# Kernel tuning notes

Measured on AMD Instinct MI355X. Metric: run time of the kernel, lower is better.

Reference implementation:

```python
import jax, jax.numpy as jnp
import numpy as np

NUM_Q_HEADS = 64
NUM_KV_HEADS = 8
HEAD_DIM = 64
HIDDEN = 2880
SLIDING_WINDOW = 128
ROPE_WAVELENGTH = 10000.0
NEG_INF = jnp.float32(-1e9)


def _rope(x, start_index=0):
    # x: (b, s, n, h). yarn with scaling_factor=1.0 == standard RoPE (split-half rotate).
    s, h = x.shape[1], x.shape[-1]
    inv_freq = 1.0 / (ROPE_WAVELENGTH ** (jnp.arange(0, h, 2, dtype=jnp.float32) / h))
    pos = jnp.arange(s, dtype=jnp.float32) + start_index
    freqs = pos[:, None] * inv_freq[None, :]  # (s, h/2)
    cos = jnp.concatenate([jnp.cos(freqs), jnp.cos(freqs)], axis=-1)[None, :, None, :]
    sin = jnp.concatenate([jnp.sin(freqs), jnp.sin(freqs)], axis=-1)[None, :, None, :]
    x1, x2 = jnp.split(x, 2, axis=-1)
    rot = jnp.concatenate([-x2, x1], axis=-1)
    return x * cos + rot * sin


def setup_inputs() -> dict:
    key = jax.random.key(0)
    ks = jax.random.split(key, 9)
    b, s = 1, 2048
    scale = 0.02
    hidden_states = jax.random.normal(ks[0], (b, s, HIDDEN), jnp.float32)
    Wq = jax.random.normal(ks[1], (HIDDEN, NUM_Q_HEADS, HEAD_DIM), jnp.float32) * scale
    Wk = jax.random.normal(ks[2], (HIDDEN, NUM_KV_HEADS, HEAD_DIM), jnp.float32) * scale
    Wv = jax.random.normal(ks[3], (HIDDEN, NUM_KV_HEADS, HEAD_DIM), jnp.float32) * scale
    Wo = jax.random.normal(ks[4], (NUM_Q_HEADS, HEAD_DIM, HIDDEN), jnp.float32) * scale
    bq = jnp.zeros((NUM_Q_HEADS, HEAD_DIM), jnp.float32)
    bk = jnp.zeros((NUM_KV_HEADS, HEAD_DIM), jnp.float32)
    bv = jnp.zeros((NUM_KV_HEADS, HEAD_DIM), jnp.float32)
    bo = jnp.zeros((HIDDEN,), jnp.float32)
    sinks = jax.random.normal(ks[5], (NUM_Q_HEADS,), jnp.float32) * 0.05
    attention_mask = jnp.tril(jnp.ones((s, s), bool))[None]  # causal, (b, q, k)
    return dict(hidden_states=hidden_states, Wq=Wq, bq=bq, Wk=Wk, bk=bk, Wv=Wv,
                bv=bv, Wo=Wo, bo=bo, sinks=sinks, attention_mask=attention_mask)


def reference(hidden_states, Wq, bq, Wk, bk, Wv, bv, Wo, bo, sinks, attention_mask):
    b, s, _ = hidden_states.shape
    inv_norm = 1.0 / np.sqrt(HEAD_DIM).astype(np.float32)
    # QKV projections (EinsumDense with bias)
    q = jnp.einsum('bqm,muh->bquh', hidden_states, Wq) + bq
    k = jnp.einsum('bkm,mvh->bkvh', hidden_states, Wk) + bk
    v = jnp.einsum('bkm,mvh->bkvh', hidden_states, Wv) + bv
    # rotary_dim == head_dim (even), so RoPE applies to the full head dim
    q = _rope(q)
    k = _rope(k)
    # GQA: repeat kv heads
    groups = NUM_Q_HEADS // NUM_KV_HEADS
    k = jnp.repeat(k, groups, axis=2)
    v = jnp.repeat(v, groups, axis=2)
    scores = jnp.einsum('bquh,bkuh->buqk', q, k) * inv_norm
    # sliding-window mask: keep kv_pos >= q_pos - window
    qpos = jnp.arange(s)
    swin = qpos[None, :] >= qpos[:, None] - SLIDING_WINDOW  # (q, k)
    scores = jnp.where(swin[None, None], scores, NEG_INF)
    scores = jnp.where(attention_mask[:, None], scores, NEG_INF)
    # sink-token logit per head appended as extra kv column
    sink = jnp.broadcast_to(sinks.reshape(1, NUM_Q_HEADS, 1, 1), (b, NUM_Q_HEADS, s, 1))
    logits = jnp.concatenate([scores, sink], axis=-1)
    m = jax.lax.stop_gradient(jnp.max(logits, axis=-1, keepdims=True))
    probs = jax.nn.softmax(logits - m, axis=-1)[..., :-1]  # drop sink column
    attn = jnp.einsum('buqk,bkuh->bquh', probs, v)
    return jnp.einsum('bquh,uhm->bqm', attn, Wo) + bo
```

## Files before the change

kernel.cpp:

```cpp
#include <hip/hip_runtime.h>
#include <cstdint>

typedef __attribute__((ext_vector_type(4))) float f32x4;
typedef __attribute__((ext_vector_type(8))) short bf16x8;

#define HIDDEN 2880
#define SEQ 2048
#define QKV_N 5120
#define WIN 128

__device__ __forceinline__ ushort f2bf(float f) {
  uint32_t u = __builtin_bit_cast(uint32_t, f);
  u += 0x7fff + ((u >> 16) & 1);
  return (ushort)(u >> 16);
}
__device__ __forceinline__ float bf2f(ushort h) {
  uint32_t u = ((uint32_t)h) << 16;
  return __builtin_bit_cast(float, u);
}

__global__ void conv_kernel(const float* __restrict__ in, ushort* __restrict__ out, int n) {
  int i = (blockIdx.x * blockDim.x + threadIdx.x) * 8;
  if (i >= n) return;
  float4 a = *(const float4*)(in + i);
  float4 b = *(const float4*)(in + i + 4);
  bf16x8 o;
  o[0] = (short)f2bf(a.x); o[1] = (short)f2bf(a.y); o[2] = (short)f2bf(a.z); o[3] = (short)f2bf(a.w);
  o[4] = (short)f2bf(b.x); o[5] = (short)f2bf(b.y); o[6] = (short)f2bf(b.z); o[7] = (short)f2bf(b.w);
  *(bf16x8*)(out + i) = o;
}

__global__ __launch_bounds__(256) void tconv2_kernel(const float* __restrict__ in, ushort* __restrict__ out,
                                                     int C, int out_ld, int out_row_off) {
  __shared__ ushort tile[64][68];
  int c0 = blockIdx.x * 64, r0 = blockIdx.y * 64;
  int t = threadIdx.x;
  int lr = t >> 4;
  int lc = (t & 15) * 4;
#pragma unroll
  for (int i = 0; i < 4; ++i) {
    float4 v = *(const float4*)&in[(size_t)(r0 + i * 16 + lr) * C + c0 + lc];
    ushort4 o;
    o.x = f2bf(v.x); o.y = f2bf(v.y); o.z = f2bf(v.z); o.w = f2bf(v.w);
    *(ushort4*)&tile[i * 16 + lr][lc] = o;
  }
  __syncthreads();
  int rr0 = (t & 7) * 8;
#pragma unroll
  for (int i2 = 0; i2 < 2; ++i2) {
    int cc = i2 * 32 + (t >> 3);
    bf16x8 o;
#pragma unroll
    for (int j = 0; j < 8; ++j) o[j] = (short)tile[rr0 + j][cc];
    *(bf16x8*)&out[(size_t)(out_row_off + c0 + cc) * out_ld + r0 + rr0] = o;
  }
}

__global__ void biascat_kernel(const float* __restrict__ bq, const float* __restrict__ bk,
                               const float* __restrict__ bv, float* __restrict__ out) {
  int i = blockIdx.x * blockDim.x + threadIdx.x;
  if (i >= QKV_N) return;
  float v = (i < 4096) ? bq[i] : (i < 4608) ? bk[i - 4096] : bv[i - 4608];
  out[i] = v;
}

__global__ void ropetab_kernel(float2* __restrict__ tab) {
  int i = blockIdx.x * blockDim.x + threadIdx.x;
  int s = i >> 5, d = i & 31;
  float inv = powf(10000.0f, -(float)d / 32.0f);
  float f = (float)s * inv;
  tab[i] = make_float2(cosf(f), sinf(f));
}

__global__ __launch_bounds__(256) void vt_kernel(const ushort* __restrict__ qkv, ushort* __restrict__ vt) {
  __shared__ ushort tile[64][80];
  int kv0 = blockIdx.x * 64, d0 = blockIdx.y * 64;
  int t = threadIdx.x;
#pragma unroll
  for (int p = 0; p < 2; ++p) {
    int lr = p * 32 + (t >> 3);
    *(bf16x8*)&tile[lr][(t & 7) * 8] =
        *(const bf16x8*)&qkv[(size_t)(kv0 + lr) * QKV_N + 4608 + d0 + (t & 7) * 8];
  }
  __syncthreads();
#pragma unroll
  for (int p = 0; p < 2; ++p) {
    int dl = p * 32 + (t >> 3);
    bf16x8 o;
#pragma unroll
    for (int jj = 0; jj < 8; ++jj) o[jj] = (short)tile[(t & 7) * 8 + jj][dl];
    *(bf16x8*)&vt[(size_t)(d0 + dl) * 2048 + kv0 + (t & 7) * 8] = o;
  }
}

template <int BN, bool OUT_BF16>
__global__ __launch_bounds__(256, 2) void gemm4w_kernel(
    const ushort* __restrict__ A, const ushort* __restrict__ Bt,
    const float* __restrict__ bias, void* __restrict__ Cv,
    int K, int lda, int ldb, int ldc) {
  constexpr int NFRAG = BN / 32;
  constexpr int BHALF = BN * 64;
  constexpr int BCHUNKS = BHALF / 1024;
  constexpr int BUFBYTES = 16384 + 2 * BHALF;
  __shared__ __align__(16) char ldsbuf[2 * BUFBYTES];

  const int cpx = gridDim.x >> 3;
  const int wg = ((int)blockIdx.x & 7) * cpx + ((int)blockIdx.x >> 3);
  const int mtile = wg & 15, ntile = wg >> 4;
  const int m0 = mtile * 128, n0 = ntile * BN;

  const int tid = threadIdx.x, wv = tid >> 6, l = tid & 63;
  const int wm = wv >> 1, wn = wv & 1;
  const int r = l & 15, g = l >> 4;

  const int c = l ^ ((l >> 3) & 3);
  const ushort* gA0 = A + (size_t)(m0 + (c >> 2)) * lda + (c & 3) * 8;
  const ushort* gB0 = Bt + (size_t)(n0 + (c >> 2)) * ldb + (c & 3) * 8;

  const int gsw = (g * 16) ^ (((r >> 1) & 3) << 4);
  const int aOff = (wm * 64 + r) * 64 + gsw;
  const int bOff = (wn * (NFRAG * 16) + r) * 64 + gsw;

  auto sA = [&](int nb, int kg, int kh) {
#pragma unroll
    for (int j = 0; j < 2; ++j) {
      int cid = j * 4 + wv;
      __builtin_amdgcn_global_load_lds(
          (const __attribute__((address_space(1))) void*)(const void*)(gA0 + (size_t)cid * 16 * lda + kg),
          (__attribute__((address_space(3))) void*)&ldsbuf[nb * BUFBYTES + kh * 8192 + cid * 1024], 16, 0, 0);
    }
  };
  auto sB = [&](int nb, int kg, int kh) {
#pragma unroll
    for (int j = 0; j < (BCHUNKS + 3) / 4; ++j) {
      int cid = j * 4 + wv;
      if (cid < BCHUNKS)
        __builtin_amdgcn_global_load_lds(
            (const __attribute__((address_space(1))) void*)(const void*)(gB0 + (size_t)cid * 16 * ldb + kg),
            (__attribute__((address_space(3))) void*)&ldsbuf[nb * BUFBYTES + 16384 + kh * BHALF + cid * 1024],
            16, 0, 0);
    }
  };

#define BAR() __builtin_amdgcn_s_barrier()
#define LGKMC(N)                                                       \
  do {                                                                 \
    asm volatile("s_waitcnt lgkmcnt(%0)" ::"n"(N) : "memory");         \
    __builtin_amdgcn_sched_barrier(0);                                 \
  } while (0)
#define WAITV0() asm volatile("s_waitcnt vmcnt(0)" ::: "memory")

  f32x4 acc[4][NFRAG] = {};
  const int nt = K >> 6;

  sA(0, 0, 0); sA(0, 32, 1); sB(0, 0, 0); sB(0, 32, 1);
  WAITV0();
  BAR();

  for (int t = 0; t < nt; ++t) {
    const int bufOff = (t & 1) * BUFBYTES;
    const int nb = (t & 1) ^ 1;
    bf16x8 aq0[4], bq0[NFRAG], aq1[4], bq1[NFRAG];
#pragma unroll
    for (int nf = 0; nf < NFRAG; ++nf)
      bq0[nf] = *(const bf16x8*)&ldsbuf[bufOff + 16384 + bOff + nf * 1024];
#pragma unroll
    for (int mi = 0; mi < 4; ++mi)
      aq0[mi] = *(const bf16x8*)&ldsbuf[bufOff + aOff + mi * 1024];
    __builtin_amdgcn_sched_barrier(0);
#pragma unroll
    for (int nf = 0; nf < NFRAG; ++nf)
      bq1[nf] = *(const bf16x8*)&ldsbuf[bufOff + 16384 + BHALF + bOff + nf * 1024];
#pragma unroll
    for (int mi = 0; mi < 4; ++mi)
      aq1[mi] = *(const bf16x8*)&ldsbuf[bufOff + 8192 + aOff + mi * 1024];
    if (t + 1 < nt) {
      const int kn = (t + 1) * 64;
      sA(nb, kn, 0); sA(nb, kn + 32, 1);
      sB(nb, kn, 0); sB(nb, kn + 32, 1);
    }
    LGKMC(4 + NFRAG);
    __builtin_amdgcn_s_setprio(1);
#pragma unroll
    for (int mi = 0; mi < 4; ++mi)
#pragma unroll
      for (int nf = 0; nf < NFRAG; ++nf)
        acc[mi][nf] = __builtin_amdgcn_mfma_f32_16x16x32_bf16(aq0[mi], bq0[nf], acc[mi][nf], 0, 0, 0);
    __builtin_amdgcn_s_setprio(0);
    LGKMC(0);
    __builtin_amdgcn_s_setprio(1);
#pragma unroll
    for (int mi = 0; mi < 4; ++mi)
#pragma unroll
      for (int nf = 0; nf < NFRAG; ++nf)
        acc[mi][nf] = __builtin_amdgcn_mfma_f32_16x16x32_bf16(aq1[mi], bq1[nf], acc[mi][nf], 0, 0, 0);
    __builtin_amdgcn_s_setprio(0);
    WAITV0();
    BAR();
  }

#pragma unroll
  for (int mf2 = 0; mf2 < 4; ++mf2) {
#pragma unroll
    for (int nf = 0; nf < NFRAG; ++nf) {
      int cc = n0 + wn * (NFRAG * 16) + nf * 16 + r;
      float b = bias[cc];
#pragma unroll
      for (int j = 0; j < 4; ++j) {
        int rrow = m0 + wm * 64 + mf2 * 16 + g * 4 + j;
        float v = acc[mf2][nf][j] + b;
        if (OUT_BF16) ((ushort*)Cv)[(size_t)rrow * ldc + cc] = f2bf(v);
        else ((float*)Cv)[(size_t)rrow * ldc + cc] = v;
      }
    }
  }
#undef BAR
#undef LGKMC
#undef WAITV0
}

__global__ __launch_bounds__(512, 4) void attn_kernel(
    const ushort* __restrict__ qkv, const ushort* __restrict__ vt,
    const float* __restrict__ sinks, const float2* __restrict__ tab,
    ushort* __restrict__ out) {
  __shared__ __align__(16) char lds[54272];
  const int kh = blockIdx.y;
  const int q0 = blockIdx.x * 32;
  const int kvw0 = q0 - 128;
  const int tid = threadIdx.x, w = tid >> 6, l = tid & 63;
  const int r = l & 15, g = l >> 4;
  const int h = kh * 8 + w;

  if (tid < 256) ((uint32_t*)(lds + 40960))[tid] = 0;

#pragma unroll
  for (int it = 0; it < 4; ++it) {
    int c = it * 512 + tid;
    if (c < 640) {
      int row = c >> 2, ch = c & 3;
      int kv = kvw0 + row;
      bf16x8 v1 = {}, v2 = {};
      if (kv >= 0) {
        const ushort* kb = &qkv[(size_t)kv * QKV_N + 4096 + kh * 64 + ch * 8];
        bf16x8 x1 = *(const bf16x8*)kb;
        bf16x8 x2 = *(const bf16x8*)(kb + 32);
#pragma unroll
        for (int i = 0; i < 8; ++i) {
          float2 cs = tab[(kv << 5) + ch * 8 + i];
          float a = bf2f((ushort)x1[i]), b = bf2f((ushort)x2[i]);
          v1[i] = (short)f2bf(a * cs.x - b * cs.y);
          v2[i] = (short)f2bf(b * cs.x + a * cs.y);
        }
      }
      int b1 = (row * 128 + ch * 16) ^ ((row & 7) << 4);
      int b2 = (row * 128 + (ch + 4) * 16) ^ ((row & 7) << 4);
      *(bf16x8*)(lds + b1) = v1;
      *(bf16x8*)(lds + b2) = v2;
    } else if (c < 1920) {
      int cv = c - 640;
      int row = cv / 20, ch = cv - (cv / 20) * 20;
      int kv = kvw0 + ch * 8;
      bf16x8 vv = {};
      if (kv >= 0) vv = *(const bf16x8*)&vt[(size_t)(kh * 64 + row) * 2048 + kv];
      int byte = (row * 320 + ch * 16) ^ ((row & 7) << 4);
      *(bf16x8*)(lds + 20480 + byte) = vv;
    }
  }
  __syncthreads();

  char* Pw = lds + 41984 + w * 1536;
  const float snk = sinks[h];

#pragma unroll
  for (int si = 0; si < 2; ++si) {
    const ushort* qb = &qkv[(size_t)(q0 + si * 16 + r) * QKV_N + h * 64 + g * 8];
    bf16x8 qf0 = *(const bf16x8*)qb;
    bf16x8 qf1 = *(const bf16x8*)(qb + 32);
    {
      int s = q0 + si * 16 + r;
      bf16x8 t0, t1;
#pragma unroll
      for (int i = 0; i < 8; ++i) {
        float2 cs = tab[(s << 5) + g * 8 + i];
        float a = bf2f((ushort)qf0[i]), b = bf2f((ushort)qf1[i]);
        t0[i] = (short)f2bf(a * cs.x - b * cs.y);
        t1[i] = (short)f2bf(b * cs.x + a * cs.y);
      }
      qf0 = t0; qf1 = t1;
    }

    f32x4 S[9];
    float mx[4] = {-3e30f, -3e30f, -3e30f, -3e30f};
#pragma unroll
    for (int tt = 0; tt < 9; ++tt) {
      int kvloc = (si + tt) * 16 + r;
      int b0 = (kvloc * 128 + g * 16) ^ ((kvloc & 7) << 4);
      int b1 = (kvloc * 128 + 64 + g * 16) ^ ((kvloc & 7) << 4);
      bf16x8 kf0 = *(const bf16x8*)(lds + b0);
      bf16x8 kf1 = *(const bf16x8*)(lds + b1);
      f32x4 s = {};
      s = __builtin_amdgcn_mfma_f32_16x16x32_bf16(qf0, kf0, s, 0, 0, 0);
      s = __builtin_amdgcn_mfma_f32_16x16x32_bf16(qf1, kf1, s, 0, 0, 0);
      int kvc = kvw0 + kvloc;
#pragma unroll
      for (int j = 0; j < 4; ++j) {
        int qr = q0 + si * 16 + g * 4 + j;
        bool valid = (kvc >= 0) && (kvc <= qr) && (kvc >= qr - WIN);
        float v = valid ? s[j] * 0.125f : -1e30f;
        s[j] = v;
        mx[j] = fmaxf(mx[j], v);
      }
      S[tt] = s;
    }
#pragma unroll
    for (int off = 1; off < 16; off <<= 1)
#pragma unroll
      for (int j = 0; j < 4; ++j) mx[j] = fmaxf(mx[j], __shfl_xor(mx[j], off, 64));
    float m[4], sum[4] = {0, 0, 0, 0};
#pragma unroll
    for (int j = 0; j < 4; ++j) m[j] = fmaxf(mx[j], snk);
#pragma unroll
    for (int tt = 0; tt < 9; ++tt)
#pragma unroll
      for (int j = 0; j < 4; ++j) {
        float p = (S[tt][j] > -1e29f) ? __expf(S[tt][j] - m[j]) : 0.0f;
        S[tt][j] = p;
        sum[j] += p;
      }
#pragma unroll
    for (int off = 1; off < 16; off <<= 1)
#pragma unroll
      for (int j = 0; j < 4; ++j) sum[j] += __shfl_xor(sum[j], off, 64);
    float rinv[4];
#pragma unroll
    for (int j = 0; j < 4; ++j) rinv[j] = 1.0f / (sum[j] + __expf(snk - m[j]));

    f32x4 acc[4] = {};
#pragma unroll
    for (int ks = 0; ks < 5; ++ks) {
#pragma unroll
      for (int c2 = 0; c2 < 2; ++c2) {
        int tt = 2 * ks + c2;
#pragma unroll
        for (int j = 0; j < 4; ++j) {
          float pv = (tt <= 8) ? S[tt][j] * rinv[j] : 0.0f;
          *(ushort*)(Pw + ((g * 4 + j) * 48 + c2 * 16 + r) * 2) = f2bf(pv);
        }
      }
      bf16x8 pa = *(const bf16x8*)(Pw + (r * 48 + g * 8) * 2);
#pragma unroll
      for (int ni = 0; ni < 4; ++ni) {
        int row = ni * 16 + r;
        int byte = (row * 320 + (si * 16 + ks * 32 + g * 8) * 2) ^ ((row & 7) << 4);
        bf16x8 vb = *(const bf16x8*)(lds + 20480 + byte);
        acc[ni] = __builtin_amdgcn_mfma_f32_16x16x32_bf16(pa, vb, acc[ni], 0, 0, 0);
      }
    }
#pragma unroll
    for (int ni = 0; ni < 4; ++ni)
#pragma unroll
      for (int j = 0; j < 4; ++j)
        out[(size_t)(q0 + si * 16 + g * 4 + j) * 4096 + h * 64 + ni * 16 + r] = f2bf(acc[ni][j]);
  }
}

extern "C" void kernel_launch(void* const* d_in, const int* in_sizes, int n_in,
                              void* d_out, int out_size, void* d_ws, size_t ws_size,
                              hipStream_t stream) {
  const float* hs = (const float*)d_in[0];
  const float* Wq = (const float*)d_in[1];
  const float* bq = (const float*)d_in[2];
  const float* Wk = (const float*)d_in[3];
  const float* bk = (const float*)d_in[4];
  const float* Wv = (const float*)d_in[5];
  const float* bv = (const float*)d_in[6];
  const float* Wo = (const float*)d_in[7];
  const float* bo = (const float*)d_in[8];
  const float* sinks = (const float*)d_in[9];
  float* out = (float*)d_out;

  char* ws = (char*)d_ws;
  ushort* hs_bf   = (ushort*)(ws + 0);
  ushort* vt_g    = (ushort*)(ws + 0);
  ushort* wqkv_t  = (ushort*)(ws + 11796480);
  ushort* attn    = (ushort*)(ws + 11796480);
  ushort* wo_t    = (ushort*)(ws + 41287680);
  ushort* qkv     = (ushort*)(ws + 66453504);
  float*  bias_all= (float*)(ws + 87425024);
  float2* tab     = (float2*)(ws + 87445504);

  conv_kernel<<<5898240 / 8 / 256, 256, 0, stream>>>(hs, hs_bf, 5898240);
  tconv2_kernel<<<dim3(64, 45), 256, 0, stream>>>(Wq, wqkv_t, 4096, 2880, 0);
  tconv2_kernel<<<dim3(8, 45), 256, 0, stream>>>(Wk, wqkv_t, 512, 2880, 4096);
  tconv2_kernel<<<dim3(8, 45), 256, 0, stream>>>(Wv, wqkv_t, 512, 2880, 4608);
  tconv2_kernel<<<dim3(45, 64), 256, 0, stream>>>(Wo, wo_t, 2880, 4096, 0);
  biascat_kernel<<<20, 256, 0, stream>>>(bq, bk, bv, bias_all);
  ropetab_kernel<<<2048 * 32 / 256, 256, 0, stream>>>(tab);

  gemm4w_kernel<160, true><<<512, 256, 0, stream>>>(hs_bf, wqkv_t, bias_all, qkv,
                                                    2880, 2880, 2880, 5120);
  vt_kernel<<<dim3(32, 8), 256, 0, stream>>>(qkv, vt_g);
  attn_kernel<<<dim3(64, 8), 512, 0, stream>>>(qkv, vt_g, sinks, tab, attn);
  gemm4w_kernel<192, false><<<240, 256, 0, stream>>>(attn, wo_t, bo, out,
                                                     4096, 4096, 4096, 2880);
}
```

Measured before the change: 202.7 us.

## Add intra-block split-K GEMM for QKV projection and retune output GEMM tiles

Adds a new 512-thread QKV projection GEMM with 128x320 tiles. Its 8 waves are split into two K-halves, and the two partial sums are reduced through LDS before the bias add and bf16 store, which halves the grid to 256 blocks of larger tiles. The output projection GEMM moves from BN=192 with 240 blocks to BN=160 with 288 blocks. The generic GEMM's inner loop is also restructured to load and compute each K-half in turn with a full LDS wait, replacing the previous partial-wait overlap. The aim is better data reuse and CU balance, at the cost of the LDS reduction step and possibly less overlap between LDS loads and MFMA.

Result: slower. 212.1 us (+4.6%).

```diff
diff --git a/kernel.cpp b/kernel.cpp
--- a/kernel.cpp
+++ b/kernel.cpp
@@ -90,6 +90,131 @@
 #pragma unroll
     for (int jj = 0; jj < 8; ++jj) o[jj] = (short)tile[(t & 7) * 8 + jj][dl];
     *(bf16x8*)&vt[(size_t)(d0 + dl) * 2048 + kv0 + (t & 7) * 8] = o;
+  }
+}
+
+#define LGKM0()                                              \
+  do {                                                       \
+    asm volatile("s_waitcnt lgkmcnt(0)" ::: "memory");       \
+    __builtin_amdgcn_sched_barrier(0);                       \
+  } while (0)
+#define WAITV0() asm volatile("s_waitcnt vmcnt(0)" ::: "memory")
+#define BAR() __builtin_amdgcn_s_barrier()
+
+__global__ __launch_bounds__(512, 2) void gemmks_kernel(
+    const ushort* __restrict__ A, const ushort* __restrict__ Bt,
+    const float* __restrict__ bias, ushort* __restrict__ Cv,
+    int K, int lda, int ldb, int ldc) {
+  constexpr int BUFBYTES = 57344;
+  __shared__ __align__(16) char ldsbuf[2 * BUFBYTES];
+
+  const int cpx = gridDim.x >> 3;
+  const int wg = ((int)blockIdx.x & 7) * cpx + ((int)blockIdx.x >> 3);
+  const int mtile = wg & 15, ntile = wg >> 4;
+  const int m0 = mtile * 128, n0 = ntile * 320;
+
+  const int tid = threadIdx.x, wv = tid >> 6, l = tid & 63;
+  const int wn = wv & 3, wk = wv >> 2;
+  const int r = l & 15, g = l >> 4;
+
+  const int c = l ^ ((l >> 3) & 3);
+  const ushort* gA0 = A + (size_t)(m0 + (c >> 2)) * lda + (c & 3) * 8;
+  const ushort* gB0 = Bt + (size_t)(n0 + (c >> 2)) * ldb + (c & 3) * 8;
+
+  const int gsw = (g * 16) ^ (((r >> 1) & 3) << 4);
+  const int aOff = r * 64 + gsw;
+  const int bOff = (wn * 80 + r) * 64 + gsw;
+
+  auto sA = [&](int nb, int kg) {
+#pragma unroll
+    for (int j = 0; j < 2; ++j) {
+      int cid = wv * 2 + j;
+      int kh = cid >> 3, rc = cid & 7;
+      __builtin_amdgcn_global_load_lds(
+          (const __attribute__((address_space(1))) void*)(const void*)(gA0 + (size_t)rc * 16 * lda + kg + kh * 32),
+          (__attribute__((address_space(3))) void*)&ldsbuf[nb * BUFBYTES + kh * 8192 + rc * 1024], 16, 0, 0);
+    }
+  };
+  auto sB = [&](int nb, int kg) {
+#pragma unroll
+    for (int j = 0; j < 5; ++j) {
+      int cid = wv * 5 + j;
+      int kh = cid / 20, cc = cid - (cid / 20) * 20;
+      __builtin_amdgcn_global_load_lds(
+          (const __attribute__((address_space(1))) void*)(const void*)(gB0 + (size_t)cc * 16 * ldb + kg + kh * 32),
+          (__attribute__((address_space(3))) void*)&ldsbuf[nb * BUFBYTES + 16384 + kh * 20480 + cc * 1024],
+          16, 0, 0);
+    }
+  };
+
+  f32x4 acc[8][5] = {};
+  const int nt = K >> 6;
+
+  sA(0, 0); sB(0, 0);
+  WAITV0();
+  BAR();
+
+  for (int t = 0; t < nt; ++t) {
+    const int bufOff = (t & 1) * BUFBYTES;
+    const int nb = (t & 1) ^ 1;
+    bf16x8 aq[8], bq[5];
+    const int khA = bufOff + wk * 8192;
+    const int khB = bufOff + 16384 + wk * 20480;
+#pragma unroll
+    for (int nf = 0; nf < 5; ++nf)
+      bq[nf] = *(const bf16x8*)&ldsbuf[khB + bOff + nf * 1024];
+#pragma unroll
+    for (int mi = 0; mi < 8; ++mi)
+      aq[mi] = *(const bf16x8*)&ldsbuf[khA + aOff + mi * 1024];
+    if (t + 1 < nt) { sA(nb, (t + 1) * 64); sB(nb, (t + 1) * 64); }
+    LGKM0();
+    __builtin_amdgcn_s_setprio(1);
+#pragma unroll
+    for (int mi = 0; mi < 8; ++mi)
+#pragma unroll
+      for (int nf = 0; nf < 5; ++nf)
+        acc[mi][nf] = __builtin_amdgcn_mfma_f32_16x16x32_bf16(aq[mi], bq[nf], acc[mi][nf], 0, 0, 0);
+    __builtin_amdgcn_s_setprio(0);
+    WAITV0();
+    BAR();
+  }
+
+#pragma unroll
+  for (int ch = 0; ch < 2; ++ch) {
+    if (wk == 1) {
+#pragma unroll
+      for (int mi = 0; mi < 4; ++mi)
+#pragma unroll
+        for (int nf = 0; nf < 5; ++nf)
+          *(f32x4*)&ldsbuf[wn * 20480 + (mi * 5 + nf) * 1024 + l * 16] = acc[ch * 4 + mi][nf];
+    }
+    __syncthreads();
+    if (wk == 0) {
+#pragma unroll
+      for (int mi = 0; mi < 4; ++mi)
+#pragma unroll
+        for (int nf = 0; nf < 5; ++nf) {
+          f32x4 o = *(const f32x4*)&ldsbuf[wn * 20480 + (mi * 5 + nf) * 1024 + l * 16];
+#pragma unroll
+          for (int j = 0; j < 4; ++j) acc[ch * 4 + mi][nf][j] += o[j];
+        }
+    }
+    __syncthreads();
+  }
+
+  if (wk == 0) {
+#pragma unroll
+    for (int mi = 0; mi < 8; ++mi)
+#pragma unroll
+      for (int nf = 0; nf < 5; ++nf) {
+        int cc = n0 + wn * 80 + nf * 16 + r;
+        float b = bias[cc];
+#pragma unroll
+        for (int j = 0; j < 4; ++j) {
+          int rrow = m0 + mi * 16 + g * 4 + j;
+          Cv[(size_t)rrow * ldc + cc] = f2bf(acc[mi][nf][j] + b);
+        }
+      }
   }
 }
 
@@ -142,14 +267,6 @@
     }
   };
 
-#define BAR() __builtin_amdgcn_s_barrier()
-#define LGKMC(N)                                                       \
-  do {                                                                 \
-    asm volatile("s_waitcnt lgkmcnt(%0)" ::"n"(N) : "memory");         \
-    __builtin_amdgcn_sched_barrier(0);                                 \
-  } while (0)
-#define WAITV0() asm volatile("s_waitcnt vmcnt(0)" ::: "memory")
-
   f32x4 acc[4][NFRAG] = {};
   const int nt = K >> 6;
 
@@ -160,41 +277,29 @@
   for (int t = 0; t < nt; ++t) {
     const int bufOff = (t & 1) * BUFBYTES;
     const int nb = (t & 1) ^ 1;
-    bf16x8 aq0[4], bq0[NFRAG], aq1[4], bq1[NFRAG];
-#pragma unroll
-    for (int nf = 0; nf < NFRAG; ++nf)
-      bq0[nf] = *(const bf16x8*)&ldsbuf[bufOff + 16384 + bOff + nf * 1024];
-#pragma unroll
-    for (int mi = 0; mi < 4; ++mi)
-      aq0[mi] = *(const bf16x8*)&ldsbuf[bufOff + aOff + mi * 1024];
-    __builtin_amdgcn_sched_barrier(0);
-#pragma unroll
-    for (int nf = 0; nf < NFRAG; ++nf)
-      bq1[nf] = *(const bf16x8*)&ldsbuf[bufOff + 16384 + BHALF + bOff + nf * 1024];
-#pragma unroll
-    for (int mi = 0; mi < 4; ++mi)
-      aq1[mi] = *(const bf16x8*)&ldsbuf[bufOff + 8192 + aOff + mi * 1024];
     if (t + 1 < nt) {
       const int kn = (t + 1) * 64;
       sA(nb, kn, 0); sA(nb, kn + 32, 1);
       sB(nb, kn, 0); sB(nb, kn + 32, 1);
     }
-    LGKMC(4 + NFRAG);
-    __builtin_amdgcn_s_setprio(1);
-#pragma unroll
-    for (int mi = 0; mi < 4; ++mi)
+#pragma unroll
+    for (int kh = 0; kh < 2; ++kh) {
+      bf16x8 aq[4], bq[NFRAG];
 #pragma unroll
       for (int nf = 0; nf < NFRAG; ++nf)
-        acc[mi][nf] = __builtin_amdgcn_mfma_f32_16x16x32_bf16(aq0[mi], bq0[nf], acc[mi][nf], 0, 0, 0);
-    __builtin_amdgcn_s_setprio(0);
-    LGKMC(0);
-    __builtin_amdgcn_s_setprio(1);
-#pragma unroll
-    for (int mi = 0; mi < 4; ++mi)
-#pragma unroll
-      for (int nf = 0; nf < NFRAG; ++nf)
-        acc[mi][nf] = __builtin_amdgcn_mfma_f32_16x16x32_bf16(aq1[mi], bq1[nf], acc[mi][nf], 0, 0, 0);
-    __builtin_amdgcn_s_setprio(0);
+        bq[nf] = *(const bf16x8*)&ldsbuf[bufOff + 16384 + kh * BHALF + bOff + nf * 1024];
+#pragma unroll
+      for (int mi = 0; mi < 4; ++mi)
+        aq[mi] = *(const bf16x8*)&ldsbuf[bufOff + kh * 8192 + aOff + mi * 1024];
+      LGKM0();
+      __builtin_amdgcn_s_setprio(1);
+#pragma unroll
+      for (int mi = 0; mi < 4; ++mi)
+#pragma unroll
+        for (int nf = 0; nf < NFRAG; ++nf)
+          acc[mi][nf] = __builtin_amdgcn_mfma_f32_16x16x32_bf16(aq[mi], bq[nf], acc[mi][nf], 0, 0, 0);
+      __builtin_amdgcn_s_setprio(0);
+    }
     WAITV0();
     BAR();
   }
@@ -214,9 +319,6 @@
       }
     }
   }
-#undef BAR
-#undef LGKMC
-#undef WAITV0
 }
 
 __global__ __launch_bounds__(512, 4) void attn_kernel(
@@ -397,10 +499,10 @@
   biascat_kernel<<<20, 256, 0, stream>>>(bq, bk, bv, bias_all);
   ropetab_kernel<<<2048 * 32 / 256, 256, 0, stream>>>(tab);
 
-  gemm4w_kernel<160, true><<<512, 256, 0, stream>>>(hs_bf, wqkv_t, bias_all, qkv,
-                                                    2880, 2880, 2880, 5120);
+  gemmks_kernel<<<256, 512, 0, stream>>>(hs_bf, wqkv_t, bias_all, qkv,
+                                         2880, 2880, 2880, 5120);
   vt_kernel<<<dim3(32, 8), 256, 0, stream>>>(qkv, vt_g);
   attn_kernel<<<dim3(64, 8), 512, 0, stream>>>(qkv, vt_g, sinks, tab, attn);
-  gemm4w_kernel<192, false><<<240, 256, 0, stream>>>(attn, wo_t, bo, out,
+  gemm4w_kernel<160, false><<<288, 256, 0, stream>>>(attn, wo_t, bo, out,
                                                      4096, 4096, 4096, 2880);
 }
```
